# Optimization experiments

Measured on AMD Instinct MI355X. Metric: run time of the kernel, lower is better.

The kernel has to match this reference:

```python
import jax, jax.numpy as jnp
import numpy as np
import math

E = 512      # embed_dim
H = 8        # num_heads
HD = E // H  # head_dim
S = 2048     # seq_len
B = 4        # batch


def setup_inputs() -> dict:
    key = jax.random.key(0)
    ks = jax.random.split(key, 8)
    std = 1.0 / math.sqrt(E)
    return {
        "query": jax.random.normal(ks[0], (S, B, E), jnp.float32),
        "key": jax.random.normal(ks[1], (S, B, E), jnp.float32),
        "value": jax.random.normal(ks[2], (S, B, E), jnp.float32),
        "relative_pos_bias": jax.random.normal(ks[3], (H, S, S), jnp.float32),
        "in_proj_weight": jax.random.normal(ks[4], (3 * E, E), jnp.float32) * std,
        "in_proj_bias": jnp.zeros((3 * E,), jnp.float32),
        "out_proj_weight": jax.random.normal(ks[5], (E, E), jnp.float32) * std,
        "out_proj_bias": jnp.zeros((E,), jnp.float32),
    }


def reference(query, key, value, relative_pos_bias,
              in_proj_weight, in_proj_bias, out_proj_weight, out_proj_bias):
    # batch_first=False: inputs are (S, B, E). Self-attn style: q,k,v all projected
    # from their respective inputs with the fused in_proj (query used for q-slice, etc.)
    wq, wk, wv = jnp.split(in_proj_weight, 3, axis=0)
    bq, bk, bv = jnp.split(in_proj_bias, 3, axis=0)
    # NOTE: original applies F.linear(q, full_in_proj) then chunks, with q==query etc.
    # Here query/key/value are distinct tensors but the torch code projects qkv from
    # the SAME tensor q (the query input). Replicate that exactly:
    qkv = query @ in_proj_weight.T + in_proj_bias          # (S, B, 3E)
    q, k, v = jnp.split(qkv, 3, axis=-1)                    # each (S, B, E)
    q = q.reshape(S, B, H, HD)
    k = k.reshape(S, B, H, HD)
    v = v.reshape(S, B, H, HD)
    scale = 1.0 / math.sqrt(HD)
    # scores: (B, H, S, S)
    scores = jnp.einsum('ibhd,jbhd->bhij', q, k) * scale
    bias = jnp.clip(relative_pos_bias, -5.0, 5.0)[None]     # (1, H, S, S)
    scores = scores + bias * 0.05
    scores = jnp.clip(scores, -30.0, 30.0)
    m = jax.lax.stop_gradient(jnp.max(scores, axis=-1, keepdims=True))
    attn_weights = jax.nn.softmax(scores - m, axis=-1)       # (B, H, S, S)
    out = jnp.einsum('bhij,jbhd->ibhd', attn_weights, v)     # (S, B, H, HD)
    out = jnp.where(jnp.isnan(out), 0.0, out)
    # torch: view(B,H,S,hd).transpose(1,2).view(B,S,E) == our (S,B,H,HD)->(B,S,E)
    out = out.transpose(1, 0, 2, 3).reshape(B, S, E)
    out = jnp.clip(out, -10.0, 10.0)
    out = out @ out_proj_weight.T + out_proj_bias            # (B, S, E)
    out = jnp.where(jnp.isnan(out), 0.0, out)
    # batch_first=False: return (S, B, E)
    return out.transpose(1, 0, 2), attn_weights
```

## Files before the change

kernel.cpp:

```cpp
#include <hip/hip_runtime.h>
#include <hip/hip_bf16.h>

#define S_LEN 2048
#define BATCH 4
#define EMB   512
#define NH    8
#define HD    64
#define SB    (S_LEN*BATCH)
#define E3    (3*EMB)
#define BH    (BATCH*NH)

typedef _Float16 f16;
typedef _Float16 f16x4 __attribute__((ext_vector_type(4)));
typedef _Float16 f16x8 __attribute__((ext_vector_type(8)));
typedef float    f32x4 __attribute__((ext_vector_type(4)));

#define LDS_FENCE() do { asm volatile("s_waitcnt lgkmcnt(0)" ::: "memory"); \
                         __builtin_amdgcn_sched_barrier(0); } while (0)

__global__ __launch_bounds__(256) void k_cast(const float* __restrict__ q,
    const float* __restrict__ wi, const float* __restrict__ wo,
    f16* __restrict__ qh, f16* __restrict__ wih, f16* __restrict__ woh)
{
    const int NQ4 = (SB*EMB)/4, NW4 = (E3*EMB)/4, NO4 = (EMB*EMB)/4;
    const int total = NQ4 + NW4 + NO4;
    for (int i = blockIdx.x * 256 + threadIdx.x; i < total; i += gridDim.x * 256) {
        const float* src; f16* dst; int j;
        if (i < NQ4)            { src = q;  dst = qh;  j = i; }
        else if (i < NQ4 + NW4) { src = wi; dst = wih; j = i - NQ4; }
        else                    { src = wo; dst = woh; j = i - NQ4 - NW4; }
        f32x4 v = *(const f32x4*)(src + (size_t)j * 4);
        f16x4 h4;
        #pragma unroll
        for (int jj = 0; jj < 4; ++jj) h4[jj] = (f16)v[jj];
        *(f16x4*)(dst + (size_t)j * 4) = h4;
    }
}

__global__ __launch_bounds__(256) void k_qkv_h(const f16* __restrict__ Ah,
    const f16* __restrict__ Bw, const float* __restrict__ bin,
    f16* __restrict__ Qh, f16* __restrict__ Kh, f16* __restrict__ Vt)
{
    __shared__ f16 As[128 * 64];
    __shared__ f16 Bs[128 * 64];
    const int tid = threadIdx.x;
    const int w = tid >> 6, l = tid & 63;
    const int g = l >> 4, li = l & 15;
    const int wm = w >> 1, wn = w & 1;
    const int row0 = blockIdx.x * 128;
    const int col0 = blockIdx.y * 128;

    const int srow = tid >> 3;
    const int sch  = tid & 7;
    const f16* ga = Ah + (size_t)(row0 + srow) * EMB + sch * 8;
    const f16* gb = Bw + (size_t)(col0 + srow) * EMB + sch * 8;

    f16x8 ra[4], rb[4];
    #pragma unroll
    for (int r = 0; r < 4; ++r) {
        ra[r] = *(const f16x8*)(ga + (size_t)r * 32 * EMB);
        rb[r] = *(const f16x8*)(gb + (size_t)r * 32 * EMB);
    }

    f32x4 acc[4][4];
    const f32x4 zero = {0.f, 0.f, 0.f, 0.f};
    #pragma unroll
    for (int m = 0; m < 4; ++m)
        #pragma unroll
        for (int n = 0; n < 4; ++n) acc[m][n] = zero;

    for (int kt = 0; kt < 8; ++kt) {
        __syncthreads();
        #pragma unroll
        for (int r = 0; r < 4; ++r) {
            const int rw = srow + 32 * r;
            const int po = rw * 64 + ((sch ^ (rw & 7)) << 3);
            *(f16x8*)&As[po] = ra[r];
            *(f16x8*)&Bs[po] = rb[r];
        }
        __syncthreads();
        if (kt < 7) {
            const int kn = (kt + 1) * 64;
            #pragma unroll
            for (int r = 0; r < 4; ++r) {
                ra[r] = *(const f16x8*)(ga + kn + (size_t)r * 32 * EMB);
                rb[r] = *(const f16x8*)(gb + kn + (size_t)r * 32 * EMB);
            }
        }
        #pragma unroll
        for (int kb = 0; kb < 2; ++kb) {
            f16x8 af[4], bf[4];
            #pragma unroll
            for (int m = 0; m < 4; ++m)
                af[m] = *(const f16x8*)&As[(wm*64 + m*16 + li) * 64 +
                                           (((kb*4 + g) ^ (li & 7)) << 3)];
            #pragma unroll
            for (int n = 0; n < 4; ++n)
                bf[n] = *(const f16x8*)&Bs[(wn*64 + n*16 + li) * 64 +
                                           (((kb*4 + g) ^ (li & 7)) << 3)];
            #pragma unroll
            for (int m = 0; m < 4; ++m)
                #pragma unroll
                for (int n = 0; n < 4; ++n)
                    acc[m][n] = __builtin_amdgcn_mfma_f32_16x16x32_f16(af[m], bf[n], acc[m][n], 0, 0, 0);
        }
    }

    #pragma unroll
    for (int n = 0; n < 4; ++n) {
        const int coln  = col0 + wn*64 + n*16 + li;
        const int which = coln >> 9;
        const int h     = (coln >> 6) & 7;
        const int d     = coln & 63;
        const float bb  = bin[coln];
        #pragma unroll
        for (int m = 0; m < 4; ++m) {
            const int rbase = row0 + wm*64 + m*16 + g*4;
            const int s = rbase >> 2;
            #pragma unroll
            for (int jj = 0; jj < 4; ++jj) {
                const float v = acc[m][n][jj] + bb;
                const int bh = jj * NH + h;
                if (which == 2)
                    Vt[((size_t)bh * HD + d) * S_LEN + s] = (f16)v;
                else
                    (which ? Kh : Qh)[((size_t)bh * S_LEN + s) * HD + d] = (f16)v;
            }
        }
    }
}

__global__ __launch_bounds__(256, 4) void k_attn(
    const f16* __restrict__ Qh, const f16* __restrict__ Kh, const f16* __restrict__ Vt,
    const float* __restrict__ rpb, float* __restrict__ att, f16* __restrict__ ctxh)
{
    __shared__ f16   KT[64*64];
    __shared__ f16   VTs[64*64];
    __shared__ float SBm[4][16*64];
    __shared__ f16   PBm[4][16*64];

    const int tid = threadIdx.x;
    const int w  = tid >> 6, l = tid & 63;
    const int g  = l >> 4, li = l & 15;
    const int l8 = l >> 3, l7 = l & 7;
    const int bx = blockIdx.x;
    const int b  = bx & 3;
    const int rt = (bx >> 2) & 31;
    const int h  = bx >> 7;
    const int bh = b * NH + h;
    const int r0 = rt * 64 + w * 16;

    const f16* qbase = Qh + ((size_t)bh * S_LEN + r0 + li) * HD;
    const f16x8 bq0 = *(const f16x8*)(qbase + g * 8);
    const f16x8 bq1 = *(const f16x8*)(qbase + 32 + g * 8);

    const int sr0 = w * 16 + l8;
    const int sr1 = sr0 + 8;
    const int scl = (l7 ^ l8) * 8;
    const f16* kg0 = Kh + ((size_t)bh * S_LEN + sr0) * HD + scl;
    const f16* kg1 = Kh + ((size_t)bh * S_LEN + sr1) * HD + scl;
    const f16* vg0 = Vt + ((size_t)bh * HD + sr0) * S_LEN + scl;
    const f16* vg1 = Vt + ((size_t)bh * HD + sr1) * S_LEN + scl;
    const int stw0 = (w * 2 + 0) * 512 + l * 8;
    const int stw1 = (w * 2 + 1) * 512 + l * 8;

    const int fK0 = li * 64 + ((g ^ (li & 7)) << 3);
    const int fK1 = li * 64 + (((g + 4) ^ (li & 7)) << 3);

    float* SBw = &SBm[w][0];
    f16*   PBw = &PBm[w][0];
    const int sbr = l8 * 64 + ((l7 ^ l8) << 2);

    const float* bias0 = rpb + ((size_t)h * S_LEN + r0 + l8) * S_LEN + l7 * 4;
    const float* bias1 = bias0 + (size_t)8 * S_LEN;
    float* att0 = att + ((size_t)bh * S_LEN + r0 + l8) * S_LEN + l7 * 4;
    float* att1 = att0 + (size_t)8 * S_LEN;

    const f32x4 zero = {0.f, 0.f, 0.f, 0.f};

    float ls0 = 0.f, ls1 = 0.f;
    f16x8 tk0 = *(const f16x8*)kg0;
    f16x8 tk1 = *(const f16x8*)kg1;
    for (int t = 0; t < 32; ++t) {
        __syncthreads();
        *(f16x8*)&KT[stw0] = tk0;
        *(f16x8*)&KT[stw1] = tk1;
        __syncthreads();
        const int tn1 = (t < 31) ? t + 1 : 31;
        tk0 = *(const f16x8*)(kg0 + (size_t)tn1 * 4096);
        tk1 = *(const f16x8*)(kg1 + (size_t)tn1 * 4096);
        #pragma unroll
        for (int half = 0; half < 2; ++half) {
            #pragma unroll
            for (int n2 = 0; n2 < 2; ++n2) {
                const int n = half * 2 + n2;
                f16x8 a0 = *(const f16x8*)&KT[n * 1024 + fK0];
                f16x8 a1 = *(const f16x8*)&KT[n * 1024 + fK1];
                f32x4 st = __builtin_amdgcn_mfma_f32_16x16x32_f16(a0, bq0, zero, 0, 0, 0);
                st = __builtin_amdgcn_mfma_f32_16x16x32_f16(a1, bq1, st, 0, 0, 0);
                *(f32x4*)&SBw[li * 64 + ((((n * 4) + g) ^ (li & 7)) << 2)] = st;
            }
            LDS_FENCE();
            #pragma unroll
            for (int i = 0; i < 2; ++i) {
                f32x4 sc = *(const f32x4*)&SBw[sbr + i * 512 + half * 32];
                f32x4 bz = *(const f32x4*)((i ? bias1 : bias0) + t * 64 + half * 32);
                float acc = 0.f;
                #pragma unroll
                for (int jj = 0; jj < 4; ++jj) {
                    float bc = fminf(fmaxf(bz[jj], -5.f), 5.f) * 0.05f;
                    float v  = sc[jj] * 0.125f + bc;
                    v = fminf(fmaxf(v, -30.f), 30.f);
                    acc += __expf(v - 30.f);
                }
                if (i) ls1 += acc; else ls0 += acc;
            }
        }
    }
    ls0 += __shfl_xor(ls0, 1); ls0 += __shfl_xor(ls0, 2); ls0 += __shfl_xor(ls0, 4);
    ls1 += __shfl_xor(ls1, 1); ls1 += __shfl_xor(ls1, 2); ls1 += __shfl_xor(ls1, 4);
    const float inv0 = 1.0f / ls0;
    const float inv1 = 1.0f / ls1;

    f32x4 o[4] = {zero, zero, zero, zero};
    tk0 = *(const f16x8*)kg0;
    tk1 = *(const f16x8*)kg1;
    f16x8 tv0 = *(const f16x8*)vg0;
    f16x8 tv1 = *(const f16x8*)vg1;
    for (int t = 0; t < 32; ++t) {
        __syncthreads();
        *(f16x8*)&KT[stw0]  = tk0;
        *(f16x8*)&KT[stw1]  = tk1;
        *(f16x8*)&VTs[stw0] = tv0;
        *(f16x8*)&VTs[stw1] = tv1;
        __syncthreads();
        const int tn1 = (t < 31) ? t + 1 : 31;
        tk0 = *(const f16x8*)(kg0 + (size_t)tn1 * 4096);
        tk1 = *(const f16x8*)(kg1 + (size_t)tn1 * 4096);
        tv0 = *(const f16x8*)(vg0 + (size_t)tn1 * 64);
        tv1 = *(const f16x8*)(vg1 + (size_t)tn1 * 64);
        #pragma unroll
        for (int half = 0; half < 2; ++half) {
            #pragma unroll
            for (int n2 = 0; n2 < 2; ++n2) {
                const int n = half * 2 + n2;
                f16x8 a0 = *(const f16x8*)&KT[n * 1024 + fK0];
                f16x8 a1 = *(const f16x8*)&KT[n * 1024 + fK1];
                f32x4 st = __builtin_amdgcn_mfma_f32_16x16x32_f16(a0, bq0, zero, 0, 0, 0);
                st = __builtin_amdgcn_mfma_f32_16x16x32_f16(a1, bq1, st, 0, 0, 0);
                *(f32x4*)&SBw[li * 64 + ((((n * 4) + g) ^ (li & 7)) << 2)] = st;
            }
            LDS_FENCE();
            #pragma unroll
            for (int i = 0; i < 2; ++i) {
                f32x4 sc = *(const f32x4*)&SBw[sbr + i * 512 + half * 32];
                f32x4 bz = *(const f32x4*)((i ? bias1 : bias0) + t * 64 + half * 32);
                const float invi = i ? inv1 : inv0;
                f32x4 w4;
                f16x4 p4;
                #pragma unroll
                for (int jj = 0; jj < 4; ++jj) {
                    float bc = fminf(fmaxf(bz[jj], -5.f), 5.f) * 0.05f;
                    float v  = sc[jj] * 0.125f + bc;
                    v = fminf(fmaxf(v, -30.f), 30.f);
                    float wt = __expf(v - 30.f) * invi;
                    w4[jj] = wt;
                    p4[jj] = (f16)wt;
                }
                __builtin_nontemporal_store(w4,
                    (f32x4*)((i ? att1 : att0) + t * 64 + half * 32));
                *(f16x4*)&PBw[(i * 8 + l8) * 64 +
                              (((half * 4 + (l7 >> 1)) ^ l8) << 3) + ((l & 1) << 2)] = p4;
            }
        }
        LDS_FENCE();
        const f16x8 pa0 = *(const f16x8*)&PBw[fK0];
        const f16x8 pa1 = *(const f16x8*)&PBw[fK1];
        #pragma unroll
        for (int n = 0; n < 4; ++n) {
            f16x8 v0 = *(const f16x8*)&VTs[n * 1024 + fK0];
            f16x8 v1 = *(const f16x8*)&VTs[n * 1024 + fK1];
            o[n] = __builtin_amdgcn_mfma_f32_16x16x32_f16(pa0, v0, o[n], 0, 0, 0);
            o[n] = __builtin_amdgcn_mfma_f32_16x16x32_f16(pa1, v1, o[n], 0, 0, 0);
        }
    }

    #pragma unroll
    for (int n = 0; n < 4; ++n) {
        #pragma unroll
        for (int jj = 0; jj < 4; ++jj) {
            const int row = r0 + g * 4 + jj;
            float v = fminf(fmaxf(o[n][jj], -10.f), 10.f);
            ctxh[((size_t)row * BATCH + b) * EMB + h * HD + n * 16 + li] = (f16)v;
        }
    }
}

__global__ __launch_bounds__(256) void k_outproj_h(const f16* __restrict__ Ah,
    const f16* __restrict__ Bw, const float* __restrict__ bout,
    float* __restrict__ out)
{
    __shared__ f16 As[128 * 64];
    __shared__ f16 Bs[128 * 64];
    const int tid = threadIdx.x;
    const int w = tid >> 6, l = tid & 63;
    const int g = l >> 4, li = l & 15;
    const int wm = w >> 1, wn = w & 1;
    const int row0 = blockIdx.x * 128;
    const int col0 = blockIdx.y * 128;

    const int srow = tid >> 3;
    const int sch  = tid & 7;
    const f16* ga = Ah + (size_t)(row0 + srow) * EMB + sch * 8;
    const f16* gb = Bw + (size_t)(col0 + srow) * EMB + sch * 8;

    f16x8 ra[4], rb[4];
    #pragma unroll
    for (int r = 0; r < 4; ++r) {
        ra[r] = *(const f16x8*)(ga + (size_t)r * 32 * EMB);
        rb[r] = *(const f16x8*)(gb + (size_t)r * 32 * EMB);
    }

    f32x4 acc[4][4];
    const f32x4 zero = {0.f, 0.f, 0.f, 0.f};
    #pragma unroll
    for (int m = 0; m < 4; ++m)
        #pragma unroll
        for (int n = 0; n < 4; ++n) acc[m][n] = zero;

    for (int kt = 0; kt < 8; ++kt) {
        __syncthreads();
        #pragma unroll
        for (int r = 0; r < 4; ++r) {
            const int rw = srow + 32 * r;
            const int po = rw * 64 + ((sch ^ (rw & 7)) << 3);
            *(f16x8*)&As[po] = ra[r];
            *(f16x8*)&Bs[po] = rb[r];
        }
        __syncthreads();
        if (kt < 7) {
            const int kn = (kt + 1) * 64;
            #pragma unroll
            for (int r = 0; r < 4; ++r) {
                ra[r] = *(const f16x8*)(ga + kn + (size_t)r * 32 * EMB);
                rb[r] = *(const f16x8*)(gb + kn + (size_t)r * 32 * EMB);
            }
        }
        #pragma unroll
        for (int kb = 0; kb < 2; ++kb) {
            f16x8 af[4], bf[4];
            #pragma unroll
            for (int m = 0; m < 4; ++m)
                af[m] = *(const f16x8*)&As[(wm*64 + m*16 + li) * 64 +
                                           (((kb*4 + g) ^ (li & 7)) << 3)];
            #pragma unroll
            for (int n = 0; n < 4; ++n)
                bf[n] = *(const f16x8*)&Bs[(wn*64 + n*16 + li) * 64 +
                                           (((kb*4 + g) ^ (li & 7)) << 3)];
            #pragma unroll
            for (int m = 0; m < 4; ++m)
                #pragma unroll
                for (int n = 0; n < 4; ++n)
                    acc[m][n] = __builtin_amdgcn_mfma_f32_16x16x32_f16(af[m], bf[n], acc[m][n], 0, 0, 0);
        }
    }

    #pragma unroll
    for (int n = 0; n < 4; ++n) {
        const int coln = col0 + wn*64 + n*16 + li;
        const float bb = bout[coln];
        #pragma unroll
        for (int m = 0; m < 4; ++m) {
            const int rbase = row0 + wm*64 + m*16 + g*4;
            #pragma unroll
            for (int jj = 0; jj < 4; ++jj)
                out[(size_t)(rbase + jj) * EMB + coln] = acc[m][n][jj] + bb;
        }
    }
}

extern "C" void kernel_launch(void* const* d_in, const int* in_sizes, int n_in,
                              void* d_out, int out_size, void* d_ws, size_t ws_size,
                              hipStream_t stream) {
    const float* query = (const float*)d_in[0];
    const float* rpb  = (const float*)d_in[3];
    const float* Win  = (const float*)d_in[4];
    const float* bin  = (const float*)d_in[5];
    const float* Wout = (const float*)d_in[6];
    const float* bout = (const float*)d_in[7];

    float* out = (float*)d_out;
    float* att = out + (size_t)S_LEN * BATCH * EMB;

    const size_t per = (size_t)BH * S_LEN * HD;
    f16* Qh    = (f16*)d_ws;
    f16* Kh    = Qh + per;
    f16* Vt    = Kh + per;
    f16* AqCtx = Vt + per;
    f16* Winh  = AqCtx + per;
    f16* Wouth = Winh + (size_t)E3 * EMB;

    k_cast     <<<dim3(2048),            256, 0, stream>>>(query, Win, Wout, AqCtx, Winh, Wouth);
    k_qkv_h    <<<dim3(SB/128, E3/128),  256, 0, stream>>>(AqCtx, Winh, bin, Qh, Kh, Vt);
    k_attn     <<<dim3(4 * 32 * NH),     256, 0, stream>>>(Qh, Kh, Vt, rpb, att, AqCtx);
    k_outproj_h<<<dim3(SB/128, EMB/128), 256, 0, stream>>>(AqCtx, Wouth, bout, out);
}
```

Before: 288.0 us.

## Write V row-major then transpose via LDS kernel; reverse attention tile order

```diff
diff --git a/kernel.cpp b/kernel.cpp
--- a/kernel.cpp
+++ b/kernel.cpp
@@ -39,7 +39,7 @@
 
 __global__ __launch_bounds__(256) void k_qkv_h(const f16* __restrict__ Ah,
     const f16* __restrict__ Bw, const float* __restrict__ bin,
-    f16* __restrict__ Qh, f16* __restrict__ Kh, f16* __restrict__ Vt)
+    f16* __restrict__ Qh, f16* __restrict__ Kh, f16* __restrict__ Vh)
 {
     __shared__ f16 As[128 * 64];
     __shared__ f16 Bs[128 * 64];
@@ -113,20 +113,47 @@
         const int h     = (coln >> 6) & 7;
         const int d     = coln & 63;
         const float bb  = bin[coln];
+        f16* base = (which == 0) ? Qh : (which == 1) ? Kh : Vh;
         #pragma unroll
         for (int m = 0; m < 4; ++m) {
             const int rbase = row0 + wm*64 + m*16 + g*4;
             const int s = rbase >> 2;
             #pragma unroll
             for (int jj = 0; jj < 4; ++jj) {
-                const float v = acc[m][n][jj] + bb;
                 const int bh = jj * NH + h;
-                if (which == 2)
-                    Vt[((size_t)bh * HD + d) * S_LEN + s] = (f16)v;
-                else
-                    (which ? Kh : Qh)[((size_t)bh * S_LEN + s) * HD + d] = (f16)v;
-            }
-        }
+                base[((size_t)bh * S_LEN + s) * HD + d] = (f16)(acc[m][n][jj] + bb);
+            }
+        }
+    }
+}
+
+__global__ __launch_bounds__(256) void k_vt(const f16* __restrict__ Vh,
+                                            f16* __restrict__ Vt)
+{
+    __shared__ f16 T[64 * 64];
+    const int tid = threadIdx.x;
+    const int l = tid & 63, w = tid >> 6;
+    const int bh = blockIdx.y;
+    const int s0 = blockIdx.x * 64;
+    const int r8 = l >> 3;
+    const int ch = l & 7;
+
+    #pragma unroll
+    for (int it = 0; it < 2; ++it) {
+        const int srow = it * 32 + w * 8 + r8;
+        f16x8 v = *(const f16x8*)&Vh[((size_t)bh * S_LEN + s0 + srow) * HD + ch * 8];
+        #pragma unroll
+        for (int i = 0; i < 8; ++i) {
+            const int d = ch * 8 + i;
+            T[d * 64 + (((srow >> 3) ^ (d & 7)) << 3) + (srow & 7)] = v[i];
+        }
+    }
+    __syncthreads();
+    #pragma unroll
+    for (int it = 0; it < 2; ++it) {
+        const int d = it * 32 + w * 8 + r8;
+        f16x8 v = *(const f16x8*)&T[d * 64 + ((ch ^ (d & 7)) << 3)];
+        *(f16x8*)&Vt[((size_t)bh * HD + d) * S_LEN + s0 + ch * 8] = v;
     }
 }
 
@@ -223,22 +250,23 @@
     const float inv1 = 1.0f / ls1;
 
     f32x4 o[4] = {zero, zero, zero, zero};
-    tk0 = *(const f16x8*)kg0;
-    tk1 = *(const f16x8*)kg1;
-    f16x8 tv0 = *(const f16x8*)vg0;
-    f16x8 tv1 = *(const f16x8*)vg1;
-    for (int t = 0; t < 32; ++t) {
+    tk0 = *(const f16x8*)(kg0 + (size_t)31 * 4096);
+    tk1 = *(const f16x8*)(kg1 + (size_t)31 * 4096);
+    f16x8 tv0 = *(const f16x8*)(vg0 + (size_t)31 * 64);
+    f16x8 tv1 = *(const f16x8*)(vg1 + (size_t)31 * 64);
+    for (int tt = 0; tt < 32; ++tt) {
+        const int t = 31 - tt;
         __syncthreads();
         *(f16x8*)&KT[stw0]  = tk0;
         *(f16x8*)&KT[stw1]  = tk1;
         *(f16x8*)&VTs[stw0] = tv0;
         *(f16x8*)&VTs[stw1] = tv1;
         __syncthreads();
-        const int tn1 = (t < 31) ? t + 1 : 31;
-        tk0 = *(const f16x8*)(kg0 + (size_t)tn1 * 4096);
-        tk1 = *(const f16x8*)(kg1 + (size_t)tn1 * 4096);
-        tv0 = *(const f16x8*)(vg0 + (size_t)tn1 * 64);
-        tv1 = *(const f16x8*)(vg1 + (size_t)tn1 * 64);
+        const int tp = (t > 0) ? t - 1 : 0;
+        tk0 = *(const f16x8*)(kg0 + (size_t)tp * 4096);
+        tk1 = *(const f16x8*)(kg1 + (size_t)tp * 4096);
+        tv0 = *(const f16x8*)(vg0 + (size_t)tp * 64);
+        tv1 = *(const f16x8*)(vg1 + (size_t)tp * 64);
         #pragma unroll
         for (int half = 0; half < 2; ++half) {
             #pragma unroll
@@ -399,9 +427,11 @@
     f16* AqCtx = Vt + per;
     f16* Winh  = AqCtx + per;
     f16* Wouth = Winh + (size_t)E3 * EMB;
+    f16* Vh    = Wouth + (size_t)EMB * EMB;
 
     k_cast     <<<dim3(2048),            256, 0, stream>>>(query, Win, Wout, AqCtx, Winh, Wouth);
-    k_qkv_h    <<<dim3(SB/128, E3/128),  256, 0, stream>>>(AqCtx, Winh, bin, Qh, Kh, Vt);
+    k_qkv_h    <<<dim3(SB/128, E3/128),  256, 0, stream>>>(AqCtx, Winh, bin, Qh, Kh, Vh);
+    k_vt       <<<dim3(S_LEN/64, BH),    256, 0, stream>>>(Vh, Vt);
     k_attn     <<<dim3(4 * 32 * NH),     256, 0, stream>>>(Qh, Kh, Vt, rpb, att, AqCtx);
     k_outproj_h<<<dim3(SB/128, EMB/128), 256, 0, stream>>>(AqCtx, Wouth, bout, out);
 }
```

New measurement: 286.3 us. About the same (-0.6%).
